# Performance work log

Measured on AMD Instinct MI355X. Metric: run time of the kernel, lower is better.

The kernel has to match this reference:

```python
import jax, jax.numpy as jnp
import numpy as np


def setup_inputs() -> dict:
    key = jax.random.key(0)
    kq, kk, kv = jax.random.split(key, 3)
    B, L, H, D = 2, 4096, 8, 64
    queries = jax.random.normal(kq, (B, L, H, D), dtype=jnp.float32)
    keys = jax.random.normal(kk, (B, L, H, D), dtype=jnp.float32)
    values = jax.random.normal(kv, (B, L, H, D), dtype=jnp.float32)
    return {"queries": queries, "keys": keys, "values": values}


def reference(queries, keys, values):
    # queries/keys/values: [B, L, H, D]
    d_model = queries.shape[-1]
    scale = 1.0 / jnp.sqrt(jnp.asarray(d_model, dtype=queries.dtype))
    # scores: [B, H, Lq, Lk]
    scores = jnp.einsum('blhd,bshd->bhls', queries, keys)
    # dropout is identity in eval mode / for deterministic reference
    A = jax.nn.softmax(scale * scores, axis=-1)
    # output: [B, Lq, H, D]
    V = jnp.einsum('bhls,bshd->blhd', A, values)
    return V
```

## Files before the change

### kernel.cpp

```cpp
#include <hip/hip_runtime.h>

#define Bn 2
#define Ln 4096
#define Hn 8
#define Dn 64
#define NTILES (Ln/64)

typedef float    f32x4 __attribute__((ext_vector_type(4)));
typedef _Float16 f16x4 __attribute__((ext_vector_type(4)));
typedef _Float16 f16x8 __attribute__((ext_vector_type(8)));

static __device__ __forceinline__ void gld16(const void* g, void* l){
    __builtin_amdgcn_global_load_lds(
        (const __attribute__((address_space(1))) unsigned int*)g,
        (__attribute__((address_space(3))) unsigned int*)l, 16, 0, 0);
}

__global__ __launch_bounds__(256)
void kprep(const float* __restrict__ Kg, _Float16* __restrict__ kp){
    int gid = blockIdx.x*256 + threadIdx.x;
    int bh  = gid >> 15;
    int rem = gid & 32767;
    int t   = rem >> 9;
    int u   = rem & 511;
    int row = u >> 3;
    int blk = (u & 7) ^ (row & 7);
    int b = bh >> 3, h = bh & 7;
    const float* src = Kg + (((size_t)b*Ln + t*64 + row)*Hn + h)*Dn + blk*8;
    float4 a = *(const float4*)src;
    float4 c = *(const float4*)(src + 4);
    f16x8 o;
    o[0]=(_Float16)a.x; o[1]=(_Float16)a.y; o[2]=(_Float16)a.z; o[3]=(_Float16)a.w;
    o[4]=(_Float16)c.x; o[5]=(_Float16)c.y; o[6]=(_Float16)c.z; o[7]=(_Float16)c.w;
    *(f16x8*)(kp + (size_t)gid*8) = o;
}

__global__ __launch_bounds__(256)
void vprep(const float* __restrict__ Vg, _Float16* __restrict__ vp){
    __shared__ float tile[64*65];
    const int t = blockIdx.x, bh = blockIdx.y, b = bh>>3, h = bh&7;
    const int tid = threadIdx.x;
#pragma unroll
    for(int i=0;i<4;++i){
        int idx = tid + i*256;
        int k = idx >> 4, d4 = (idx & 15)*4;
        float4 v = *(const float4*)(Vg + (((size_t)b*Ln + t*64 + k)*Hn + h)*Dn + d4);
        tile[k*65 + d4+0]=v.x; tile[k*65+d4+1]=v.y;
        tile[k*65 + d4+2]=v.z; tile[k*65+d4+3]=v.w;
    }
    __syncthreads();
#pragma unroll
    for(int i=0;i<2;++i){
        int u = tid + i*256;
        int d = u >> 3;
        int kblk = (u & 7) ^ (d & 7);
        f16x8 o;
#pragma unroll
        for(int j=0;j<8;++j) o[j] = (_Float16)tile[(kblk*8+j)*65 + d];
        *(f16x8*)(vp + ((size_t)(bh*64 + t)*512 + u)*8) = o;
    }
}

__global__ __launch_bounds__(256,2)
void attn_fwd(const float* __restrict__ Qg, float* __restrict__ Og,
              const _Float16* __restrict__ kp, const _Float16* __restrict__ vp){
    __shared__ __align__(16) _Float16 sK[4096];
    __shared__ __align__(16) _Float16 sV[4096];

    const int tid  = threadIdx.x;
    const int lane = tid & 63, wv = tid >> 6;
    const int ln15 = lane & 15, lg = lane >> 4, ln7 = ln15 & 7;
    const int lgh = lg >> 1, lgl = lg & 1;
    const int bh = blockIdx.x, b = bh>>3, h = bh&7;
    const int q0 = blockIdx.y*128 + wv*32;

    const float c = 0.125f * 1.4426950408889634f;

    f16x8 qf[2][2];
#pragma unroll
    for(int qt=0;qt<2;++qt){
        const float* qrow = Qg + (((size_t)b*Ln + q0 + qt*16 + ln15)*Hn + h)*Dn;
#pragma unroll
        for(int ch=0;ch<2;++ch){
            const float* p4 = qrow + ch*32 + lg*8;
            float4 x = *(const float4*)p4;
            float4 y = *(const float4*)(p4+4);
            f16x8 f;
            f[0]=(_Float16)(x.x*c); f[1]=(_Float16)(x.y*c);
            f[2]=(_Float16)(x.z*c); f[3]=(_Float16)(x.w*c);
            f[4]=(_Float16)(y.x*c); f[5]=(_Float16)(y.y*c);
            f[6]=(_Float16)(y.z*c); f[7]=(_Float16)(y.w*c);
            qf[qt][ch]=f;
        }
    }

    f32x4 o[2][4];
    f32x4 lac[2];
#pragma unroll
    for(int qt=0;qt<2;++qt){
        lac[qt] = (f32x4){0.f,0.f,0.f,0.f};
#pragma unroll
        for(int dt=0;dt<4;++dt) o[qt][dt] = (f32x4){0.f,0.f,0.f,0.f};
    }

    const _Float16* kg = kp + ((size_t)bh*262144 + (size_t)(wv*128 + lane)*8);
    const _Float16* vg = vp + ((size_t)bh*262144 + (size_t)(wv*128 + lane)*8);
    _Float16* lK0 = sK + (size_t)(wv*128      + lane)*8;
    _Float16* lK1 = sK + (size_t)(wv*128 + 64 + lane)*8;
    _Float16* lV0 = sV + (size_t)(wv*128      + lane)*8;
    _Float16* lV1 = sV + (size_t)(wv*128 + 64 + lane)*8;

    const int kb0 = ln15*128 + (((0+lg) ^ ln7) << 4);
    const int kb1 = ln15*128 + (((4+lg) ^ ln7) << 4);
    int vb[4];
#pragma unroll
    for(int g=0; g<4; ++g)
        vb[g] = ln15*128 + (((g*2 + lgh) ^ ln7) << 4) + lgl*8;

    for(int t=0; t<NTILES; ++t){
        gld16(kg,       lK0);
        gld16(kg + 512, lK1);
        gld16(vg,       lV0);
        gld16(vg + 512, lV1);
        kg += 4096; vg += 4096;
        __syncthreads();

#pragma unroll
        for(int g=0; g<4; ++g){
            f16x8 kf0 = *(const f16x8*)((const char*)sK + g*2048 + kb0);
            f16x8 kf1 = *(const f16x8*)((const char*)sK + g*2048 + kb1);
            f16x4 vf[4];
#pragma unroll
            for(int dt=0;dt<4;++dt)
                vf[dt] = *(const f16x4*)((const char*)sV + dt*2048 + vb[g]);

#pragma unroll
            for(int qt=0;qt<2;++qt){
                f32x4 s = (f32x4){0.f,0.f,0.f,0.f};
                s = __builtin_amdgcn_mfma_f32_16x16x32_f16(kf0, qf[qt][0], s, 0,0,0);
                s = __builtin_amdgcn_mfma_f32_16x16x32_f16(kf1, qf[qt][1], s, 0,0,0);
                f32x4 p;
                p[0] = __builtin_amdgcn_exp2f(s[0]);
                p[1] = __builtin_amdgcn_exp2f(s[1]);
                p[2] = __builtin_amdgcn_exp2f(s[2]);
                p[3] = __builtin_amdgcn_exp2f(s[3]);
                lac[qt] += p;
                f16x4 pa;
                pa[0]=(_Float16)p[0]; pa[1]=(_Float16)p[1];
                pa[2]=(_Float16)p[2]; pa[3]=(_Float16)p[3];
#pragma unroll
                for(int dt=0;dt<4;++dt)
                    o[qt][dt] = __builtin_amdgcn_mfma_f32_16x16x16f16(pa, vf[dt], o[qt][dt], 0,0,0);
            }
        }
        __syncthreads();
    }

#pragma unroll
    for(int qt=0;qt<2;++qt){
        float l = (lac[qt][0]+lac[qt][1]) + (lac[qt][2]+lac[qt][3]);
        l += __shfl_xor(l, 16, 64);
        l += __shfl_xor(l, 32, 64);
        float inv = 1.0f/l;
        float invr[4];
#pragma unroll
        for(int r=0;r<4;++r) invr[r] = __shfl(inv, lg*4 + r, 64);
        float* ob = Og + (((size_t)b*Ln + q0 + qt*16)*Hn + h)*Dn;
#pragma unroll
        for(int dt=0;dt<4;++dt)
#pragma unroll
            for(int r=0;r<4;++r)
                ob[(size_t)(lg*4+r)*Hn*Dn + dt*16 + ln15] = o[qt][dt][r]*invr[r];
    }
}

extern "C" void kernel_launch(void* const* d_in, const int* in_sizes, int n_in,
                              void* d_out, int out_size, void* d_ws, size_t ws_size,
                              hipStream_t stream) {
    const float* Q = (const float*)d_in[0];
    const float* K = (const float*)d_in[1];
    const float* V = (const float*)d_in[2];
    float* O = (float*)d_out;

    _Float16* kp = (_Float16*)d_ws;
    _Float16* vp = (_Float16*)((char*)d_ws + (8u<<20));

    kprep<<<dim3(2048), dim3(256), 0, stream>>>(K, kp);
    vprep<<<dim3(64, 16), dim3(256), 0, stream>>>(V, vp);
    attn_fwd<<<dim3(16, 32), dim3(256), 0, stream>>>(Q, O, kp, vp);
}
```

Measured before the change: 178.8 us.

## Double-buffer K/V tiles, widen per-wave query tile, fuse K/V prep kernels

The attention kernel now uses 2 waves per block, each handling 64 query rows instead of 32. This increases reuse of each K/V fragment read from shared memory. K/V tiles are double-buffered in LDS, so the next tile's global-to-LDS loads run during the current tile's compute, and only one barrier is needed per iteration. The V pre-layout is reordered so each lane reads one 16-byte fragment per tile and splits it with shuffles. The separate K and V prep kernels are merged into one launch. The cost is higher register pressure and fewer resident waves per CU, which may limit latency hiding.

```diff
diff --git a/kernel.cpp b/kernel.cpp
--- a/kernel.cpp
+++ b/kernel.cpp
@@ -5,6 +5,7 @@
 #define Hn 8
 #define Dn 64
 #define NTILES (Ln/64)
+#define BH_STRIDE 262144
 
 typedef float    f32x4 __attribute__((ext_vector_type(4)));
 typedef _Float16 f16x4 __attribute__((ext_vector_type(4)));
@@ -17,29 +18,25 @@
 }
 
 __global__ __launch_bounds__(256)
-void kprep(const float* __restrict__ Kg, _Float16* __restrict__ kp){
-    int gid = blockIdx.x*256 + threadIdx.x;
-    int bh  = gid >> 15;
-    int rem = gid & 32767;
-    int t   = rem >> 9;
-    int u   = rem & 511;
-    int row = u >> 3;
-    int blk = (u & 7) ^ (row & 7);
-    int b = bh >> 3, h = bh & 7;
-    const float* src = Kg + (((size_t)b*Ln + t*64 + row)*Hn + h)*Dn + blk*8;
-    float4 a = *(const float4*)src;
-    float4 c = *(const float4*)(src + 4);
-    f16x8 o;
-    o[0]=(_Float16)a.x; o[1]=(_Float16)a.y; o[2]=(_Float16)a.z; o[3]=(_Float16)a.w;
-    o[4]=(_Float16)c.x; o[5]=(_Float16)c.y; o[6]=(_Float16)c.z; o[7]=(_Float16)c.w;
-    *(f16x8*)(kp + (size_t)gid*8) = o;
-}
-
-__global__ __launch_bounds__(256)
-void vprep(const float* __restrict__ Vg, _Float16* __restrict__ vp){
+void kvprep(const float* __restrict__ Kg, const float* __restrict__ Vg,
+            _Float16* __restrict__ kp, _Float16* __restrict__ vp){
     __shared__ float tile[64*65];
     const int t = blockIdx.x, bh = blockIdx.y, b = bh>>3, h = bh&7;
     const int tid = threadIdx.x;
+
+#pragma unroll
+    for(int i=0;i<2;++i){
+        int u = tid + i*256;
+        int row = u>>3, blk = (u&7) ^ (row&7);
+        const float* src = Kg + (((size_t)b*Ln + t*64 + row)*Hn + h)*Dn + blk*8;
+        float4 a = *(const float4*)src;
+        float4 c = *(const float4*)(src + 4);
+        f16x8 o;
+        o[0]=(_Float16)a.x; o[1]=(_Float16)a.y; o[2]=(_Float16)a.z; o[3]=(_Float16)a.w;
+        o[4]=(_Float16)c.x; o[5]=(_Float16)c.y; o[6]=(_Float16)c.z; o[7]=(_Float16)c.w;
+        *(f16x8*)(kp + (size_t)bh*BH_STRIDE + t*4096 + (size_t)u*8) = o;
+    }
+
 #pragma unroll
     for(int i=0;i<4;++i){
         int idx = tid + i*256;
@@ -49,36 +46,41 @@
         tile[k*65 + d4+2]=v.z; tile[k*65+d4+3]=v.w;
     }
     __syncthreads();
+
 #pragma unroll
     for(int i=0;i<2;++i){
         int u = tid + i*256;
-        int d = u >> 3;
-        int kblk = (u & 7) ^ (d & 7);
+        int d = u>>3, s = u&7;
+        int x = s ^ (d&7);
+        int lg = x>>1, gh = x&1;
         f16x8 o;
 #pragma unroll
-        for(int j=0;j<8;++j) o[j] = (_Float16)tile[(kblk*8+j)*65 + d];
-        *(f16x8*)(vp + ((size_t)(bh*64 + t)*512 + u)*8) = o;
-    }
-}
-
-__global__ __launch_bounds__(256,2)
+        for(int j2=0;j2<8;++j2){
+            int g = gh*2 + (j2>>2), j = j2&3;
+            int k = g*16 + lg*4 + j;
+            o[j2] = (_Float16)tile[k*65 + d];
+        }
+        *(f16x8*)(vp + (size_t)bh*BH_STRIDE + t*4096 + (size_t)u*8) = o;
+    }
+}
+
+__global__ __launch_bounds__(128,1)
 void attn_fwd(const float* __restrict__ Qg, float* __restrict__ Og,
               const _Float16* __restrict__ kp, const _Float16* __restrict__ vp){
-    __shared__ __align__(16) _Float16 sK[4096];
-    __shared__ __align__(16) _Float16 sV[4096];
+    __shared__ __align__(16) _Float16 sK[2][4096];
+    __shared__ __align__(16) _Float16 sV[2][4096];
 
     const int tid  = threadIdx.x;
     const int lane = tid & 63, wv = tid >> 6;
     const int ln15 = lane & 15, lg = lane >> 4, ln7 = ln15 & 7;
-    const int lgh = lg >> 1, lgl = lg & 1;
     const int bh = blockIdx.x, b = bh>>3, h = bh&7;
-    const int q0 = blockIdx.y*128 + wv*32;
+    const int q0 = blockIdx.y*128 + wv*64;
 
     const float c = 0.125f * 1.4426950408889634f;
 
-    f16x8 qf[2][2];
-#pragma unroll
-    for(int qt=0;qt<2;++qt){
+    f16x8 qf[4][2];
+#pragma unroll
+    for(int qt=0;qt<4;++qt){
         const float* qrow = Qg + (((size_t)b*Ln + q0 + qt*16 + ln15)*Hn + h)*Dn;
 #pragma unroll
         for(int ch=0;ch<2;++ch){
@@ -94,48 +96,60 @@
         }
     }
 
-    f32x4 o[2][4];
-    f32x4 lac[2];
-#pragma unroll
-    for(int qt=0;qt<2;++qt){
+    f32x4 o[4][4];
+    f32x4 lac[4];
+#pragma unroll
+    for(int qt=0;qt<4;++qt){
         lac[qt] = (f32x4){0.f,0.f,0.f,0.f};
 #pragma unroll
         for(int dt=0;dt<4;++dt) o[qt][dt] = (f32x4){0.f,0.f,0.f,0.f};
     }
 
-    const _Float16* kg = kp + ((size_t)bh*262144 + (size_t)(wv*128 + lane)*8);
-    const _Float16* vg = vp + ((size_t)bh*262144 + (size_t)(wv*128 + lane)*8);
-    _Float16* lK0 = sK + (size_t)(wv*128      + lane)*8;
-    _Float16* lK1 = sK + (size_t)(wv*128 + 64 + lane)*8;
-    _Float16* lV0 = sV + (size_t)(wv*128      + lane)*8;
-    _Float16* lV1 = sV + (size_t)(wv*128 + 64 + lane)*8;
+    const _Float16* kg = kp + (size_t)bh*BH_STRIDE;
+    const _Float16* vg = vp + (size_t)bh*BH_STRIDE;
 
     const int kb0 = ln15*128 + (((0+lg) ^ ln7) << 4);
     const int kb1 = ln15*128 + (((4+lg) ^ ln7) << 4);
-    int vb[4];
-#pragma unroll
-    for(int g=0; g<4; ++g)
-        vb[g] = ln15*128 + (((g*2 + lgh) ^ ln7) << 4) + lgl*8;
+    int vbofs[2];
+#pragma unroll
+    for(int gh=0; gh<2; ++gh)
+        vbofs[gh] = ln15*128 + (((lg*2+gh) ^ ln7) << 4);
+
+#pragma unroll
+    for(int i=0;i<4;++i){
+        int u = wv*256 + i*64 + lane;
+        gld16(kg + (size_t)u*8, &sK[0][(size_t)u*8]);
+        gld16(vg + (size_t)u*8, &sV[0][(size_t)u*8]);
+    }
 
     for(int t=0; t<NTILES; ++t){
-        gld16(kg,       lK0);
-        gld16(kg + 512, lK1);
-        gld16(vg,       lV0);
-        gld16(vg + 512, lV1);
-        kg += 4096; vg += 4096;
         __syncthreads();
+        const int cur = t & 1;
+        if(t+1 < NTILES){
+            const int nxt = cur ^ 1;
+            const _Float16* kgn = kg + (size_t)(t+1)*4096;
+            const _Float16* vgn = vg + (size_t)(t+1)*4096;
+#pragma unroll
+            for(int i=0;i<4;++i){
+                int u = wv*256 + i*64 + lane;
+                gld16(kgn + (size_t)u*8, &sK[nxt][(size_t)u*8]);
+                gld16(vgn + (size_t)u*8, &sV[nxt][(size_t)u*8]);
+            }
+        }
+
+        f16x8 W[4][2];
+#pragma unroll
+        for(int dt=0;dt<4;++dt)
+#pragma unroll
+            for(int gh=0;gh<2;++gh)
+                W[dt][gh] = *(const f16x8*)((const char*)&sV[cur][0] + dt*2048 + vbofs[gh]);
 
 #pragma unroll
         for(int g=0; g<4; ++g){
-            f16x8 kf0 = *(const f16x8*)((const char*)sK + g*2048 + kb0);
-            f16x8 kf1 = *(const f16x8*)((const char*)sK + g*2048 + kb1);
-            f16x4 vf[4];
-#pragma unroll
-            for(int dt=0;dt<4;++dt)
-                vf[dt] = *(const f16x4*)((const char*)sV + dt*2048 + vb[g]);
-
-#pragma unroll
-            for(int qt=0;qt<2;++qt){
+            f16x8 kf0 = *(const f16x8*)((const char*)&sK[cur][0] + g*2048 + kb0);
+            f16x8 kf1 = *(const f16x8*)((const char*)&sK[cur][0] + g*2048 + kb1);
+#pragma unroll
+            for(int qt=0;qt<4;++qt){
                 f32x4 s = (f32x4){0.f,0.f,0.f,0.f};
                 s = __builtin_amdgcn_mfma_f32_16x16x32_f16(kf0, qf[qt][0], s, 0,0,0);
                 s = __builtin_amdgcn_mfma_f32_16x16x32_f16(kf1, qf[qt][1], s, 0,0,0);
@@ -149,15 +163,19 @@
                 pa[0]=(_Float16)p[0]; pa[1]=(_Float16)p[1];
                 pa[2]=(_Float16)p[2]; pa[3]=(_Float16)p[3];
 #pragma unroll
-                for(int dt=0;dt<4;++dt)
-                    o[qt][dt] = __builtin_amdgcn_mfma_f32_16x16x16f16(pa, vf[dt], o[qt][dt], 0,0,0);
+                for(int dt=0;dt<4;++dt){
+                    f16x8 Wd = W[dt][g>>1];
+                    f16x4 vf = (g & 1)
+                        ? __builtin_shufflevector(Wd, Wd, 4,5,6,7)
+                        : __builtin_shufflevector(Wd, Wd, 0,1,2,3);
+                    o[qt][dt] = __builtin_amdgcn_mfma_f32_16x16x16f16(pa, vf, o[qt][dt], 0,0,0);
+                }
             }
         }
-        __syncthreads();
-    }
-
-#pragma unroll
-    for(int qt=0;qt<2;++qt){
+    }
+
+#pragma unroll
+    for(int qt=0;qt<4;++qt){
         float l = (lac[qt][0]+lac[qt][1]) + (lac[qt][2]+lac[qt][3]);
         l += __shfl_xor(l, 16, 64);
         l += __shfl_xor(l, 32, 64);
@@ -185,7 +203,6 @@
     _Float16* kp = (_Float16*)d_ws;
     _Float16* vp = (_Float16*)((char*)d_ws + (8u<<20));
 
-    kprep<<<dim3(2048), dim3(256), 0, stream>>>(K, kp);
-    vprep<<<dim3(64, 16), dim3(256), 0, stream>>>(V, vp);
-    attn_fwd<<<dim3(16, 32), dim3(256), 0, stream>>>(Q, O, kp, vp);
-}
+    kvprep<<<dim3(64, 16), dim3(256), 0, stream>>>(K, V, kp, vp);
+    attn_fwd<<<dim3(16, 32), dim3(128), 0, stream>>>(Q, O, kp, vp);
+}
```

Result: slower. 261.6 us (+46.3%).
